# Kernel tuning notes

Hardware: AMD Instinct MI355X
Metric: run time of the kernel (lower is better)

## Reference

```python
import jax, jax.numpy as jnp
import numpy as np

C = 512

def _conv1x1(x, w, b):
    # x: [B, C, T], w: [O, C], b: [O] -> [B, O, T]
    return jnp.einsum('oc,bct->bot', w, x) + b[None, :, None]

def setup_inputs() -> dict:
    key = jax.random.key(0)
    ks = jax.random.split(key, 9)
    B, T = 8, 2048
    s = 1.0 / np.sqrt(C)
    inp = {'x': jax.random.normal(ks[0], (B, C, T), dtype=jnp.float32)}
    names = ['theta', 'phi', 'g', 'w']
    for i, n in enumerate(names):
        inp[f'w_{n}'] = jax.random.uniform(ks[1 + 2 * i], (C, C), jnp.float32, -s, s)
        inp[f'b_{n}'] = jax.random.uniform(ks[2 + 2 * i], (C,), jnp.float32, -s, s)
    return inp

def reference(x, w_theta, b_theta, w_phi, b_phi, w_g, b_g, w_w, b_w):
    relu = jax.nn.relu
    feat_theta = relu(_conv1x1(x, w_theta, b_theta))          # [B, C, T]
    feat_phi = relu(_conv1x1(x, w_phi, b_phi))                # [B, C, T]
    # scores: Q^T K over channel dim -> [B, T, T]
    scores = jnp.einsum('bci,bcj->bij', feat_theta, feat_phi)
    attn = jax.nn.softmax(scores, axis=2)                     # [B, T, T]
    feat_g = relu(_conv1x1(x, w_g, b_g))                      # [B, C, T]
    # attention-weighted V: [B, T, T] x [B, T, C] -> [B, T, C] -> [B, C, T]
    feature = jnp.einsum('bij,bcj->bci', attn, feat_g)
    w_feature = relu(_conv1x1(feature, w_w, b_w))
    return w_feature + x
```

## Files before the change

### kernel.cpp

```cpp
#include <hip/hip_runtime.h>
#include <math.h>

#define C_DIM 512
#define T_DIM 2048
#define B_DIM 8

typedef _Float16 f16;
typedef __attribute__((ext_vector_type(8))) _Float16 half8;
typedef __attribute__((ext_vector_type(4))) _Float16 half4;
typedef __attribute__((ext_vector_type(4))) float floatx4;

typedef __attribute__((address_space(1))) void gvoid;
typedef __attribute__((address_space(3))) void lvoid;

__device__ __forceinline__ void gl_lds16(const f16* g, f16* l) {
    __builtin_amdgcn_global_load_lds((gvoid*)g, (lvoid*)l, 16, 0, 0);
}

__global__ __launch_bounds__(256) void convert_w_kernel(
    const float* __restrict__ w0, const float* __restrict__ w1,
    const float* __restrict__ w2, const float* __restrict__ w3,
    f16* __restrict__ o0, f16* __restrict__ o1,
    f16* __restrict__ o2, f16* __restrict__ o3)
{
    const float* src; f16* dst;
    switch (blockIdx.z) {
        case 0:  src = w0; dst = o0; break;
        case 1:  src = w1; dst = o1; break;
        case 2:  src = w2; dst = o2; break;
        default: src = w3; dst = o3; break;
    }
    const int idx = (blockIdx.x * 256 + threadIdx.x) * 4;
    const float4 v = *(const float4*)(src + idx);
    half4 h; h[0] = (f16)v.x; h[1] = (f16)v.y; h[2] = (f16)v.z; h[3] = (f16)v.w;
    *(half4*)(dst + idx) = h;
}

__global__ __launch_bounds__(256) void transpose_x_kernel(
    const float* __restrict__ x, f16* __restrict__ xt)
{
    __shared__ float xs[32][33];
    const int b  = blockIdx.z;
    const int t0 = blockIdx.x * 32, c0 = blockIdx.y * 32;
    const float* xb = x + (size_t)b * C_DIM * T_DIM;
    const int r = threadIdx.x >> 3, q = threadIdx.x & 7;

    const float4 v = *(const float4*)(xb + (size_t)(c0 + r) * T_DIM + t0 + q * 4);
    xs[r][q * 4 + 0] = v.x; xs[r][q * 4 + 1] = v.y;
    xs[r][q * 4 + 2] = v.z; xs[r][q * 4 + 3] = v.w;
    __syncthreads();

    f16* xtb = xt + (size_t)b * C_DIM * T_DIM;
    half4 h;
    h[0] = (f16)xs[q * 4 + 0][r]; h[1] = (f16)xs[q * 4 + 1][r];
    h[2] = (f16)xs[q * 4 + 2][r]; h[3] = (f16)xs[q * 4 + 3][r];
    *(half4*)(xtb + (size_t)(t0 + r) * C_DIM + c0 + q * 4) = h;
}

template<int MODE>
__global__ __launch_bounds__(256) void gemm_tn(
    const f16* __restrict__ A, size_t sA, int lda,
    const f16* __restrict__ B, size_t sB, int ldb,
    void* __restrict__ Cp, size_t sC, int ldc,
    const float* __restrict__ bias,
    const float* __restrict__ resid, size_t sR,
    int K)
{
    __shared__ __align__(16) f16 As[128 * 32];
    __shared__ __align__(16) f16 Bs[128 * 32];

    const int gx = gridDim.x;
    const int flat = blockIdx.y * gx + blockIdx.x;
    const int jsc = gx >> 2;
    const int sh = (jsc == 1) ? 0 : ((jsc == 4) ? 2 : (31 - __builtin_clz(jsc)));
    const int s = flat >> 4, rem = flat & 15;
    const int i0 = ((s >> sh) * 4 + (rem >> 2)) * 128;
    const int j0 = ((s & (jsc - 1)) * 4 + (rem & 3)) * 128;

    const int bz = blockIdx.z;
    A += (size_t)bz * sA;
    B += (size_t)bz * sB;

    const int tid  = threadIdx.x;
    const int lane = tid & 63;
    const int wave = tid >> 6;
    const int wy = wave >> 1, wx = wave & 1;
    const int quad = lane >> 4, l16 = lane & 15;

    const int cb0 = wave * 128,      cb1 = wave * 128 + 64;
    const int r0  = (cb0 + lane) >> 2, r1 = (cb1 + lane) >> 2;
    const int q0  = ((cb0 + lane) & 3) ^ (r0 & 3);
    const int q1  = ((cb1 + lane) & 3) ^ (r1 & 3);

    const f16* gA0 = A + (size_t)(i0 + r0) * lda + q0 * 8;
    const f16* gA1 = A + (size_t)(i0 + r1) * lda + q1 * 8;
    const f16* gB0 = B + (size_t)(j0 + r0) * ldb + q0 * 8;
    const f16* gB1 = B + (size_t)(j0 + r1) * ldb + q1 * 8;
    f16* lA0 = As + cb0 * 8;
    f16* lA1 = As + cb1 * 8;
    f16* lB0 = Bs + cb0 * 8;
    f16* lB1 = Bs + cb1 * 8;

    const int xa = (quad ^ (l16 & 3)) << 3;

    floatx4 acc[4][4] = {};

    for (int k0 = 0; k0 < K; k0 += 32) {
        __syncthreads();
        gl_lds16(gA0 + k0, lA0);
        gl_lds16(gA1 + k0, lA1);
        gl_lds16(gB0 + k0, lB0);
        gl_lds16(gB1 + k0, lB1);
        __syncthreads();

        half8 af[4], bf[4];
        #pragma unroll
        for (int mi = 0; mi < 4; ++mi)
            af[mi] = *(const half8*)&As[(wy * 64 + mi * 16 + l16) * 32 + xa];
        #pragma unroll
        for (int ni = 0; ni < 4; ++ni)
            bf[ni] = *(const half8*)&Bs[(wx * 64 + ni * 16 + l16) * 32 + xa];
        #pragma unroll
        for (int mi = 0; mi < 4; ++mi)
            #pragma unroll
            for (int ni = 0; ni < 4; ++ni)
                acc[mi][ni] = __builtin_amdgcn_mfma_f32_16x16x32_f16(
                    af[mi], bf[ni], acc[mi][ni], 0, 0, 0);
    }

    #pragma unroll
    for (int mi = 0; mi < 4; ++mi) {
        #pragma unroll
        for (int ni = 0; ni < 4; ++ni) {
            const int col = j0 + wx * 64 + ni * 16 + l16;
            #pragma unroll
            for (int r = 0; r < 4; ++r) {
                const int row = i0 + wy * 64 + mi * 16 + quad * 4 + r;
                float v = acc[mi][ni][r];
                if (MODE == 1) { v += bias[col]; v = v > 0.f ? v : 0.f; }
                if (MODE == 2) { v += bias[row]; v = v > 0.f ? v : 0.f; }
                if (MODE == 3) {
                    v += bias[row];
                    v = v > 0.f ? v : 0.f;
                    v += resid[(size_t)bz * sR + (size_t)row * ldc + col];
                    ((float*)Cp)[(size_t)bz * sC + (size_t)row * ldc + col] = v;
                } else {
                    ((f16*)Cp)[(size_t)bz * sC + (size_t)row * ldc + col] = (f16)v;
                }
            }
        }
    }
}

__global__ __launch_bounds__(256) void softmax_f16_kernel(f16* __restrict__ S)
{
    f16* p = S + (size_t)blockIdx.x * T_DIM;
    const int tid = threadIdx.x;

    half8 hv = *((const half8*)p + tid);
    float v[8];
    float lmax = -1e30f;
    #pragma unroll
    for (int c = 0; c < 8; ++c) { v[c] = (float)hv[c]; lmax = fmaxf(lmax, v[c]); }
    #pragma unroll
    for (int off = 32; off; off >>= 1)
        lmax = fmaxf(lmax, __shfl_down(lmax, off));
    __shared__ float redm[4];
    if ((tid & 63) == 0) redm[tid >> 6] = lmax;
    __syncthreads();
    const float m = fmaxf(fmaxf(redm[0], redm[1]), fmaxf(redm[2], redm[3]));

    float lsum = 0.f;
    #pragma unroll
    for (int c = 0; c < 8; ++c) { v[c] = __expf(v[c] - m); lsum += v[c]; }
    #pragma unroll
    for (int off = 32; off; off >>= 1)
        lsum += __shfl_down(lsum, off);
    __shared__ float reds[4];
    if ((tid & 63) == 0) reds[tid >> 6] = lsum;
    __syncthreads();
    const float inv = 1.f / (reds[0] + reds[1] + reds[2] + reds[3]);

    #pragma unroll
    for (int c = 0; c < 8; ++c) hv[c] = (f16)(v[c] * inv);
    *((half8*)p + tid) = hv;
}

extern "C" void kernel_launch(void* const* d_in, const int* in_sizes, int n_in,
                              void* d_out, int out_size, void* d_ws, size_t ws_size,
                              hipStream_t stream)
{
    const float* x       = (const float*)d_in[0];
    const float* w_theta = (const float*)d_in[1];
    const float* b_theta = (const float*)d_in[2];
    const float* w_phi   = (const float*)d_in[3];
    const float* b_phi   = (const float*)d_in[4];
    const float* w_g     = (const float*)d_in[5];
    const float* b_g     = (const float*)d_in[6];
    const float* w_w     = (const float*)d_in[7];
    const float* b_w     = (const float*)d_in[8];
    float* out = (float*)d_out;

    const size_t FE = (size_t)B_DIM * C_DIM * T_DIM;
    const size_t TC = (size_t)T_DIM * C_DIM;
    const size_t TT = (size_t)T_DIM * T_DIM;

    f16* xt       = (f16*)d_ws;
    f16* wt       = xt + FE;
    f16* wtheta_h = wt;
    f16* wphi_h   = wt + 262144;
    f16* wg_h     = wt + 524288;
    f16* ww_h     = wt + 786432;
    f16* theta    = wt + 1048576;
    f16* phi      = theta + FE;
    f16* g        = phi + FE;
    f16* scores   = g + FE;
    f16* feature  = theta;

    const dim3 blk(256);

    convert_w_kernel<<<dim3(256, 1, 4), blk, 0, stream>>>(
        w_theta, w_phi, w_g, w_w, wtheta_h, wphi_h, wg_h, ww_h);
    transpose_x_kernel<<<dim3(T_DIM / 32, C_DIM / 32, B_DIM), blk, 0, stream>>>(x, xt);

    gemm_tn<1><<<dim3(C_DIM / 128, T_DIM / 128, B_DIM), blk, 0, stream>>>(
        xt, TC, C_DIM, wtheta_h, 0, C_DIM, theta, TC, C_DIM, b_theta, nullptr, 0, C_DIM);
    gemm_tn<1><<<dim3(C_DIM / 128, T_DIM / 128, B_DIM), blk, 0, stream>>>(
        xt, TC, C_DIM, wphi_h, 0, C_DIM, phi, TC, C_DIM, b_phi, nullptr, 0, C_DIM);
    gemm_tn<2><<<dim3(T_DIM / 128, C_DIM / 128, B_DIM), blk, 0, stream>>>(
        wg_h, 0, C_DIM, xt, TC, C_DIM, g, TC, T_DIM, b_g, nullptr, 0, C_DIM);
    gemm_tn<0><<<dim3(T_DIM / 128, T_DIM / 128, B_DIM), blk, 0, stream>>>(
        theta, TC, C_DIM, phi, TC, C_DIM, scores, TT, T_DIM, nullptr, nullptr, 0, C_DIM);
    softmax_f16_kernel<<<dim3(B_DIM * T_DIM), blk, 0, stream>>>(scores);
    gemm_tn<0><<<dim3(C_DIM / 128, T_DIM / 128, B_DIM), blk, 0, stream>>>(
        scores, TT, T_DIM, g, TC, T_DIM, feature, TC, C_DIM, nullptr, nullptr, 0, T_DIM);
    gemm_tn<3><<<dim3(T_DIM / 128, C_DIM / 128, B_DIM), blk, 0, stream>>>(
        ww_h, 0, C_DIM, feature, TC, C_DIM, out, TC, T_DIM, b_w, x, TC, C_DIM);
}
```

Before: 312.4 us.

## Double-buffer GEMM LDS tiles and fuse theta/phi projections into one GEMM

The GEMM main loop now uses two LDS buffers and issues the global-to-LDS loads for the next K tile before computing on the current one. This removes one barrier per iteration and lets load latency overlap with MFMA work. Separately, the theta and phi weights and biases are concatenated so both projections run as one wider GEMM writing an interleaved [T,1024] buffer, and the scores GEMM reads it with stride 1024. This saves a launch and a second pass over xt, at the cost of doubled LDS use (lower occupancy) and a tile-swizzle change for non-power-of-four grid widths. The double buffering relies on the next iteration's barrier to ensure the async loads are visible, with no explicit vmcnt wait, which may be fragile.

```diff
diff --git a/kernel.cpp b/kernel.cpp
--- a/kernel.cpp
+++ b/kernel.cpp
@@ -36,6 +36,14 @@
     *(half4*)(dst + idx) = h;
 }
 
+__global__ __launch_bounds__(256) void concat_bias_kernel(
+    const float* __restrict__ b0, const float* __restrict__ b1,
+    float* __restrict__ o)
+{
+    const int i = blockIdx.x * 256 + threadIdx.x;
+    o[i] = (i < 512) ? b0[i] : b1[i - 512];
+}
+
 __global__ __launch_bounds__(256) void transpose_x_kernel(
     const float* __restrict__ x, f16* __restrict__ xt)
 {
@@ -66,16 +74,16 @@
     const float* __restrict__ resid, size_t sR,
     int K)
 {
-    __shared__ __align__(16) f16 As[128 * 32];
-    __shared__ __align__(16) f16 Bs[128 * 32];
+    __shared__ __align__(16) f16 As[2][128 * 32];
+    __shared__ __align__(16) f16 Bs[2][128 * 32];
 
     const int gx = gridDim.x;
     const int flat = blockIdx.y * gx + blockIdx.x;
     const int jsc = gx >> 2;
-    const int sh = (jsc == 1) ? 0 : ((jsc == 4) ? 2 : (31 - __builtin_clz(jsc)));
+    const int sh = (jsc <= 1) ? 0 : (31 - __builtin_clz(jsc));
     const int s = flat >> 4, rem = flat & 15;
     const int i0 = ((s >> sh) * 4 + (rem >> 2)) * 128;
-    const int j0 = ((s & (jsc - 1)) * 4 + (rem & 3)) * 128;
+    const int j0 = (((jsc <= 1) ? 0 : (s & (jsc - 1))) * 4 + (rem & 3)) * 128;
 
     const int bz = blockIdx.z;
     A += (size_t)bz * sA;
@@ -96,30 +104,34 @@
     const f16* gA1 = A + (size_t)(i0 + r1) * lda + q1 * 8;
     const f16* gB0 = B + (size_t)(j0 + r0) * ldb + q0 * 8;
     const f16* gB1 = B + (size_t)(j0 + r1) * ldb + q1 * 8;
-    f16* lA0 = As + cb0 * 8;
-    f16* lA1 = As + cb1 * 8;
-    f16* lB0 = Bs + cb0 * 8;
-    f16* lB1 = Bs + cb1 * 8;
 
     const int xa = (quad ^ (l16 & 3)) << 3;
 
     floatx4 acc[4][4] = {};
 
+    gl_lds16(gA0, &As[0][cb0 * 8]);
+    gl_lds16(gA1, &As[0][cb1 * 8]);
+    gl_lds16(gB0, &Bs[0][cb0 * 8]);
+    gl_lds16(gB1, &Bs[0][cb1 * 8]);
+
     for (int k0 = 0; k0 < K; k0 += 32) {
+        const int p = (k0 >> 5) & 1;
         __syncthreads();
-        gl_lds16(gA0 + k0, lA0);
-        gl_lds16(gA1 + k0, lA1);
-        gl_lds16(gB0 + k0, lB0);
-        gl_lds16(gB1 + k0, lB1);
-        __syncthreads();
+        if (k0 + 32 < K) {
+            const int pn = p ^ 1;
+            gl_lds16(gA0 + k0 + 32, &As[pn][cb0 * 8]);
+            gl_lds16(gA1 + k0 + 32, &As[pn][cb1 * 8]);
+            gl_lds16(gB0 + k0 + 32, &Bs[pn][cb0 * 8]);
+            gl_lds16(gB1 + k0 + 32, &Bs[pn][cb1 * 8]);
+        }
 
         half8 af[4], bf[4];
         #pragma unroll
         for (int mi = 0; mi < 4; ++mi)
-            af[mi] = *(const half8*)&As[(wy * 64 + mi * 16 + l16) * 32 + xa];
+            af[mi] = *(const half8*)&As[p][(wy * 64 + mi * 16 + l16) * 32 + xa];
         #pragma unroll
         for (int ni = 0; ni < 4; ++ni)
-            bf[ni] = *(const half8*)&Bs[(wx * 64 + ni * 16 + l16) * 32 + xa];
+            bf[ni] = *(const half8*)&Bs[p][(wx * 64 + ni * 16 + l16) * 32 + xa];
         #pragma unroll
         for (int mi = 0; mi < 4; ++mi)
             #pragma unroll
@@ -205,32 +217,31 @@
     const size_t TC = (size_t)T_DIM * C_DIM;
     const size_t TT = (size_t)T_DIM * T_DIM;
 
-    f16* xt       = (f16*)d_ws;
-    f16* wt       = xt + FE;
-    f16* wtheta_h = wt;
-    f16* wphi_h   = wt + 262144;
-    f16* wg_h     = wt + 524288;
-    f16* ww_h     = wt + 786432;
-    f16* theta    = wt + 1048576;
-    f16* phi      = theta + FE;
-    f16* g        = phi + FE;
-    f16* scores   = g + FE;
-    f16* feature  = theta;
+    f16* xt      = (f16*)d_ws;
+    f16* wtp     = xt + FE;
+    f16* wg_h    = wtp + 524288;
+    f16* ww_h    = wg_h + 262144;
+    float* btp   = (float*)(ww_h + 262144);
+    f16* tp      = (f16*)(btp + 1024);
+    f16* g       = tp + (size_t)B_DIM * T_DIM * 1024;
+    f16* scores  = g + FE;
+    f16* feature = tp;
 
     const dim3 blk(256);
 
     convert_w_kernel<<<dim3(256, 1, 4), blk, 0, stream>>>(
-        w_theta, w_phi, w_g, w_w, wtheta_h, wphi_h, wg_h, ww_h);
+        w_theta, w_phi, w_g, w_w, wtp, wtp + 262144, wg_h, ww_h);
+    concat_bias_kernel<<<dim3(4), blk, 0, stream>>>(b_theta, b_phi, btp);
     transpose_x_kernel<<<dim3(T_DIM / 32, C_DIM / 32, B_DIM), blk, 0, stream>>>(x, xt);
 
-    gemm_tn<1><<<dim3(C_DIM / 128, T_DIM / 128, B_DIM), blk, 0, stream>>>(
-        xt, TC, C_DIM, wtheta_h, 0, C_DIM, theta, TC, C_DIM, b_theta, nullptr, 0, C_DIM);
-    gemm_tn<1><<<dim3(C_DIM / 128, T_DIM / 128, B_DIM), blk, 0, stream>>>(
-        xt, TC, C_DIM, wphi_h, 0, C_DIM, phi, TC, C_DIM, b_phi, nullptr, 0, C_DIM);
+    gemm_tn<1><<<dim3(1024 / 128, T_DIM / 128, B_DIM), blk, 0, stream>>>(
+        xt, TC, C_DIM, wtp, 0, C_DIM, tp, (size_t)T_DIM * 1024, 1024,
+        btp, nullptr, 0, C_DIM);
     gemm_tn<2><<<dim3(T_DIM / 128, C_DIM / 128, B_DIM), blk, 0, stream>>>(
         wg_h, 0, C_DIM, xt, TC, C_DIM, g, TC, T_DIM, b_g, nullptr, 0, C_DIM);
     gemm_tn<0><<<dim3(T_DIM / 128, T_DIM / 128, B_DIM), blk, 0, stream>>>(
-        theta, TC, C_DIM, phi, TC, C_DIM, scores, TT, T_DIM, nullptr, nullptr, 0, C_DIM);
+        tp, (size_t)T_DIM * 1024, 1024, tp + 512, (size_t)T_DIM * 1024, 1024,
+        scores, TT, T_DIM, nullptr, nullptr, 0, C_DIM);
     softmax_f16_kernel<<<dim3(B_DIM * T_DIM), blk, 0, stream>>>(scores);
     gemm_tn<0><<<dim3(C_DIM / 128, T_DIM / 128, B_DIM), blk, 0, stream>>>(
         scores, TT, T_DIM, g, TC, T_DIM, feature, TC, C_DIM, nullptr, nullptr, 0, T_DIM);
```

Measured after the change: 298.1 us. 4.6% less time.
